# Optimization experiments

Measured on AMD Instinct MI355X. Metric: run time of the kernel, lower is better.

The kernel has to match this reference:

```python
import math
import jax, jax.numpy as jnp
import numpy as np

D_MODEL = 1024
NUM_HEADS = 16
D_HEAD = D_MODEL // NUM_HEADS  # 64
K_S = 32  # sparse top-k keys kept per query
B, N = 2, 2048


def setup_inputs() -> dict:
    key = jax.random.key(0)
    ks = jax.random.split(key, 9)
    s = 1.0 / math.sqrt(D_MODEL)
    return {
        "x": jax.random.normal(ks[0], (B, N, D_MODEL), dtype=jnp.float32),
        "Wq": jax.random.normal(ks[1], (D_MODEL, D_MODEL), dtype=jnp.float32) * s,
        "bq": jnp.zeros((D_MODEL,), dtype=jnp.float32),
        "Wk": jax.random.normal(ks[2], (D_MODEL, D_MODEL), dtype=jnp.float32) * s,
        "bk": jnp.zeros((D_MODEL,), dtype=jnp.float32),
        "Wv": jax.random.normal(ks[3], (D_MODEL, D_MODEL), dtype=jnp.float32) * s,
        "bv": jnp.zeros((D_MODEL,), dtype=jnp.float32),
        "Wo": jax.random.normal(ks[4], (D_MODEL, D_MODEL), dtype=jnp.float32) * s,
        "bo": jnp.zeros((D_MODEL,), dtype=jnp.float32),
    }


def _attn(x, Wq, bq, Wk, bk, Wv, bv, Wo, bo):
    b, n, _ = x.shape
    # projections (torch Linear: y = x W^T + b)
    q = (x @ Wq.T + bq).reshape(b, n, NUM_HEADS, D_HEAD).transpose(0, 2, 1, 3)
    k = (x @ Wk.T + bk).reshape(b, n, NUM_HEADS, D_HEAD).transpose(0, 2, 1, 3)
    v = (x @ Wv.T + bv).reshape(b, n, NUM_HEADS, D_HEAD).transpose(0, 2, 1, 3)
    # full scores [b, H, n, n]
    scores = jnp.einsum("bhqd,bhkd->bhqk", q, k) / math.sqrt(D_HEAD)
    # causal mask (triu above diagonal -> -inf)
    causal = jnp.triu(jnp.ones((n, n), dtype=bool), k=1)
    neg_inf = jnp.array(-jnp.inf, dtype=scores.dtype)
    scores = jnp.where(causal, neg_inf, scores)
    # sparse top-k: keep only K_S largest scores per query row
    vals, idx = jax.lax.top_k(scores, K_S)
    masked = jnp.full_like(scores, -jnp.inf)
    masked = jnp.put_along_axis(masked, idx, vals, axis=-1, inplace=False)
    attn = jax.nn.softmax(masked, axis=-1)  # dropout p=0.0 -> identity
    out = jnp.einsum("bhqk,bhkd->bhqd", attn, v)
    out = out.transpose(0, 2, 1, 3).reshape(b, n, D_MODEL)
    y = out @ Wo.T + bo
    return y, attn.mean(axis=1)


def reference(x, Wq, bq, Wk, bk, Wv, bv, Wo, bo):
    return _attn(x, Wq, bq, Wk, bk, Wv, bv, Wo, bo)
```

## Files before the change

### kernel.cpp

```cpp
#include <hip/hip_runtime.h>
#include <hip/hip_bf16.h>
#include <math.h>

#define BATCH   2
#define NTOK    2048
#define DMODEL  1024
#define HEADS   16
#define DHEAD   64
#define KSEL    32
#define MROWS   (BATCH * NTOK)
#define NBLK8   (NTOK / 8)
#define TPW     4

typedef short     bf16x8 __attribute__((ext_vector_type(8)));
typedef float     f32x4  __attribute__((ext_vector_type(4)));
typedef unsigned short ushort_t;
typedef unsigned long long u64;

#define GLOAD_LDS16(g, l) \
    __builtin_amdgcn_global_load_lds((const __attribute__((address_space(1))) void*)(g), \
                                     (__attribute__((address_space(3))) void*)(l), 16, 0, 0)

__device__ __forceinline__ ushort_t f2bf(float f) {
    unsigned u = __float_as_uint(f);
    unsigned r = (u + 0x7FFFu + ((u >> 16) & 1u)) >> 16;
    return (ushort_t)r;
}
__device__ __forceinline__ float bf2f(ushort_t h) {
    return __uint_as_float(((unsigned)h) << 16);
}

__device__ __forceinline__ void conv_body(const float* __restrict__ in,
                                          ushort_t* __restrict__ hi,
                                          ushort_t* __restrict__ lo, int n, int i)
{
    if (i + 3 < n) {
        const float4 v = *(const float4*)(in + i);
        ushort4 ph, pl;
        ph.x = f2bf(v.x); pl.x = f2bf(v.x - bf2f(ph.x));
        ph.y = f2bf(v.y); pl.y = f2bf(v.y - bf2f(ph.y));
        ph.z = f2bf(v.z); pl.z = f2bf(v.z - bf2f(ph.z));
        ph.w = f2bf(v.w); pl.w = f2bf(v.w - bf2f(ph.w));
        *(ushort4*)(hi + i) = ph;
        *(ushort4*)(lo + i) = pl;
    }
}

__global__ __launch_bounds__(256) void conv_split(const float* __restrict__ in,
                                                  ushort_t* __restrict__ hi,
                                                  ushort_t* __restrict__ lo, int n)
{
    const int i = (blockIdx.x * 256 + threadIdx.x) * 4;
    conv_body(in, hi, lo, n, i);
}

__global__ __launch_bounds__(256) void conv_split4(const float* __restrict__ i0, ushort_t* __restrict__ h0, ushort_t* __restrict__ l0,
                                                   const float* __restrict__ i1, ushort_t* __restrict__ h1, ushort_t* __restrict__ l1,
                                                   const float* __restrict__ i2, ushort_t* __restrict__ h2, ushort_t* __restrict__ l2,
                                                   const float* __restrict__ i3, ushort_t* __restrict__ h3, ushort_t* __restrict__ l3,
                                                   int n)
{
    const int w = blockIdx.y;
    const float* in = (w == 0) ? i0 : (w == 1) ? i1 : (w == 2) ? i2 : i3;
    ushort_t* hi = (w == 0) ? h0 : (w == 1) ? h1 : (w == 2) ? h2 : h3;
    ushort_t* lo = (w == 0) ? l0 : (w == 1) ? l1 : (w == 2) ? l2 : l3;
    const int i = (blockIdx.x * 256 + threadIdx.x) * 4;
    conv_body(in, hi, lo, n, i);
}

__device__ __forceinline__ unsigned mono_key(float f) {
    const unsigned u = __float_as_uint(f);
    return (u ^ (unsigned)(((int)u >> 31) | 0x80000000)) + 1u;
}
__device__ __forceinline__ float unmono(unsigned m) {
    const unsigned u = m - 1u;
    return __uint_as_float(u ^ (unsigned)(((int)(~u) >> 31) | 0x80000000));
}

__global__ __launch_bounds__(256, 2) void gemm_qkv_fused(const ushort_t* __restrict__ xhi,
                                                         const ushort_t* __restrict__ xlo,
                                                         const ushort_t* __restrict__ wqh,
                                                         const ushort_t* __restrict__ wql,
                                                         const ushort_t* __restrict__ wkh,
                                                         const ushort_t* __restrict__ wkl,
                                                         const ushort_t* __restrict__ wvh,
                                                         const ushort_t* __restrict__ wvl,
                                                         const float* __restrict__ bq,
                                                         const float* __restrict__ bk,
                                                         const float* __restrict__ bv,
                                                         ushort_t* __restrict__ Qh,
                                                         ushort_t* __restrict__ Qm,
                                                         ushort_t* __restrict__ Ql,
                                                         ushort_t* __restrict__ Kh,
                                                         ushort_t* __restrict__ Km,
                                                         ushort_t* __restrict__ Kl,
                                                         float* __restrict__ Vws)
{
    __shared__ ushort_t smem[2 * 20480];

    const int tid  = threadIdx.x;
    const int wave = tid >> 6;
    const int lane = tid & 63;
    const int fr   = lane & 15;
    const int k8   = lane >> 4;
    const int m0 = blockIdx.x * 128;
    const int n0 = blockIdx.y * 64;

    f32x4 acc[3][2][4];
#pragma unroll
    for (int w = 0; w < 3; ++w)
#pragma unroll
        for (int i = 0; i < 2; ++i)
#pragma unroll
            for (int j = 0; j < 4; ++j) acc[w][i][j] = (f32x4){0.f, 0.f, 0.f, 0.f};

#define STAGEF(bufsel, k0v) do {                                               \
        ushort_t* dst_ = smem + (size_t)(bufsel) * 20480;                      \
        _Pragma("unroll")                                                      \
        for (int i_ = 0; i_ < 2; ++i_) {                                       \
            const int c_ = i_ * 256 + tid;                                     \
            const int row_ = c_ >> 2;                                          \
            const int g_ = (c_ & 3) ^ ((row_ >> 1) & 3);                       \
            const size_t ga_ = (size_t)(m0 + row_) * DMODEL + (k0v) + g_ * 8;  \
            GLOAD_LDS16(xhi + ga_, dst_ + (size_t)c_ * 8);                     \
            GLOAD_LDS16(xlo + ga_, dst_ + 4096 + (size_t)c_ * 8);              \
        }                                                                      \
        {                                                                      \
            const int c_ = tid;                                                \
            const int row_ = c_ >> 2;                                          \
            const int g_ = (c_ & 3) ^ ((row_ >> 1) & 3);                       \
            const size_t gb_ = (size_t)(n0 + row_) * DMODEL + (k0v) + g_ * 8;  \
            GLOAD_LDS16(wqh + gb_, dst_ + 8192 + (size_t)c_ * 8);              \
            GLOAD_LDS16(wql + gb_, dst_ + 10240 + (size_t)c_ * 8);             \
            GLOAD_LDS16(wkh + gb_, dst_ + 12288 + (size_t)c_ * 8);             \
            GLOAD_LDS16(wkl + gb_, dst_ + 14336 + (size_t)c_ * 8);             \
            GLOAD_LDS16(wvh + gb_, dst_ + 16384 + (size_t)c_ * 8);             \
            GLOAD_LDS16(wvl + gb_, dst_ + 18432 + (size_t)c_ * 8);             \
        }                                                                      \
    } while (0)

    STAGEF(0, 0);
    int cur = 0;

    for (int k0 = 0; k0 < DMODEL; k0 += 32) {
        __syncthreads();
        if (k0 + 32 < DMODEL) STAGEF(cur ^ 1, k0 + 32);

        const ushort_t* buf = smem + (size_t)cur * 20480;
        bf16x8 afh[2], afl[2];
#pragma unroll
        for (int mi = 0; mi < 2; ++mi) {
            const int r = wave * 32 + mi * 16 + fr;
            const int ro = r * 32 + (k8 ^ ((r >> 1) & 3)) * 8;
            afh[mi] = *(const bf16x8*)(buf + ro);
            afl[mi] = *(const bf16x8*)(buf + 4096 + ro);
        }

#pragma unroll
        for (int w = 0; w < 3; ++w) {
            const ushort_t* bb = buf + 8192 + w * 4096;
            bf16x8 bfh[4], bfl[4];
#pragma unroll
            for (int ni = 0; ni < 4; ++ni) {
                const int r = ni * 16 + fr;
                const int ro = r * 32 + (k8 ^ ((r >> 1) & 3)) * 8;
                bfh[ni] = *(const bf16x8*)(bb + ro);
                bfl[ni] = *(const bf16x8*)(bb + 2048 + ro);
            }
#pragma unroll
            for (int mi = 0; mi < 2; ++mi)
#pragma unroll
                for (int ni = 0; ni < 4; ++ni) {
                    acc[w][mi][ni] = __builtin_amdgcn_mfma_f32_16x16x32_bf16(afh[mi], bfl[ni], acc[w][mi][ni], 0, 0, 0);
                    acc[w][mi][ni] = __builtin_amdgcn_mfma_f32_16x16x32_bf16(afl[mi], bfh[ni], acc[w][mi][ni], 0, 0, 0);
                    acc[w][mi][ni] = __builtin_amdgcn_mfma_f32_16x16x32_bf16(afh[mi], bfh[ni], acc[w][mi][ni], 0, 0, 0);
                }
        }
        cur ^= 1;
    }
#undef STAGEF

#pragma unroll
    for (int w = 0; w < 3; ++w) {
        const float* bias = (w == 0) ? bq : (w == 1) ? bk : bv;
        ushort_t* oh = (w == 0) ? Qh : Kh;
        ushort_t* om = (w == 0) ? Qm : Km;
        ushort_t* ol = (w == 0) ? Ql : Kl;
#pragma unroll
        for (int ni = 0; ni < 4; ++ni) {
            const int o = n0 + ni * 16 + (lane & 15);
            const float bvv = bias[o];
            const int hd = o >> 6;
            const int d  = o & 63;
#pragma unroll
            for (int mi = 0; mi < 2; ++mi) {
#pragma unroll
                for (int reg = 0; reg < 4; ++reg) {
                    const int m = m0 + wave * 32 + mi * 16 + ((lane >> 4) << 2) + reg;
                    const float v = acc[w][mi][ni][reg] + bvv;
                    const int bb = m >> 11;
                    const int n  = m & 2047;
                    const size_t off = (((size_t)(bb * HEADS + hd)) * NTOK + n) * DHEAD + d;
                    if (w == 2) {
                        Vws[off] = v;
                    } else {
                        const ushort_t h1 = f2bf(v);
                        const float r1 = v - bf2f(h1);
                        const ushort_t m1 = f2bf(r1);
                        const ushort_t l1 = f2bf(r1 - bf2f(m1));
                        oh[off] = h1; om[off] = m1; ol[off] = l1;
                    }
                }
            }
        }
    }
}

__global__ __launch_bounds__(256, 2) void gemm_split_mfma(const ushort_t* __restrict__ Ahi,
                                                          const ushort_t* __restrict__ Alo,
                                                          const ushort_t* __restrict__ Bhi,
                                                          const ushort_t* __restrict__ Blo,
                                                          const float* __restrict__ bias,
                                                          float* __restrict__ out)
{
    __shared__ ushort_t smem[2 * 12288];

    const int tid  = threadIdx.x;
    const int wave = tid >> 6;
    const int lane = tid & 63;
    const int fr   = lane & 15;
    const int k8   = lane >> 4;
    const int m0 = blockIdx.x * 128;
    const int n0 = blockIdx.y * 64;

    f32x4 acc[2][4];
#pragma unroll
    for (int i = 0; i < 2; ++i)
#pragma unroll
        for (int j = 0; j < 4; ++j) acc[i][j] = (f32x4){0.f, 0.f, 0.f, 0.f};

#define STAGE(bufsel, k0v) do {                                                \
        ushort_t* dst_ = smem + (size_t)(bufsel) * 12288;                      \
        _Pragma("unroll")                                                      \
        for (int i_ = 0; i_ < 2; ++i_) {                                       \
            const int c_ = i_ * 256 + tid;                                     \
            const int row_ = c_ >> 2;                                          \
            const int g_ = (c_ & 3) ^ ((row_ >> 1) & 3);                       \
            const size_t ga_ = (size_t)(m0 + row_) * DMODEL + (k0v) + g_ * 8;  \
            GLOAD_LDS16(Ahi + ga_, dst_ + (size_t)c_ * 8);                     \
            GLOAD_LDS16(Alo + ga_, dst_ + 4096 + (size_t)c_ * 8);              \
        }                                                                      \
        {                                                                      \
            const int c_ = tid;                                                \
            const int row_ = c_ >> 2;                                          \
            const int g_ = (c_ & 3) ^ ((row_ >> 1) & 3);                       \
            const size_t gb_ = (size_t)(n0 + row_) * DMODEL + (k0v) + g_ * 8;  \
            GLOAD_LDS16(Bhi + gb_, dst_ + 8192 + (size_t)c_ * 8);              \
            GLOAD_LDS16(Blo + gb_, dst_ + 10240 + (size_t)c_ * 8);             \
        }                                                                      \
    } while (0)

    STAGE(0, 0);
    int cur = 0;

    for (int k0 = 0; k0 < DMODEL; k0 += 32) {
        __syncthreads();
        if (k0 + 32 < DMODEL) STAGE(cur ^ 1, k0 + 32);

        const ushort_t* buf = smem + (size_t)cur * 12288;
        bf16x8 afh[2], afl[2], bfh[4], bfl[4];
#pragma unroll
        for (int mi = 0; mi < 2; ++mi) {
            const int r = wave * 32 + mi * 16 + fr;
            const int ro = r * 32 + (k8 ^ ((r >> 1) & 3)) * 8;
            afh[mi] = *(const bf16x8*)(buf + ro);
            afl[mi] = *(const bf16x8*)(buf + 4096 + ro);
        }
#pragma unroll
        for (int ni = 0; ni < 4; ++ni) {
            const int r = ni * 16 + fr;
            const int ro = r * 32 + (k8 ^ ((r >> 1) & 3)) * 8;
            bfh[ni] = *(const bf16x8*)(buf + 8192 + ro);
            bfl[ni] = *(const bf16x8*)(buf + 10240 + ro);
        }

#pragma unroll
        for (int mi = 0; mi < 2; ++mi)
#pragma unroll
            for (int ni = 0; ni < 4; ++ni) {
                acc[mi][ni] = __builtin_amdgcn_mfma_f32_16x16x32_bf16(afh[mi], bfl[ni], acc[mi][ni], 0, 0, 0);
                acc[mi][ni] = __builtin_amdgcn_mfma_f32_16x16x32_bf16(afl[mi], bfh[ni], acc[mi][ni], 0, 0, 0);
                acc[mi][ni] = __builtin_amdgcn_mfma_f32_16x16x32_bf16(afh[mi], bfh[ni], acc[mi][ni], 0, 0, 0);
            }
        cur ^= 1;
    }
#undef STAGE

#pragma unroll
    for (int ni = 0; ni < 4; ++ni) {
        const int o = n0 + ni * 16 + (lane & 15);
        const float bv = bias[o];
#pragma unroll
        for (int mi = 0; mi < 2; ++mi) {
#pragma unroll
            for (int reg = 0; reg < 4; ++reg) {
                const int m = m0 + wave * 32 + mi * 16 + ((lane >> 4) << 2) + reg;
                out[(size_t)m * DMODEL + o] = acc[mi][ni][reg] + bv;
            }
        }
    }
}

__global__ __launch_bounds__(256, 3) void score_mfma(const ushort_t* __restrict__ Qh,
                                                     const ushort_t* __restrict__ Qm,
                                                     const ushort_t* __restrict__ Ql,
                                                     const ushort_t* __restrict__ Kh,
                                                     const ushort_t* __restrict__ Km,
                                                     const ushort_t* __restrict__ Kl,
                                                     unsigned* __restrict__ S,
                                                     unsigned* __restrict__ Smax,
                                                     int q0, int QC)
{
    const int ks = blockIdx.x;
    const int qt = blockIdx.y;
    const int bh = blockIdx.z;
    const int qbase = q0 + qt * 128;
    const int ktmax = ((qbase + 127) >> 6) + 1;
    const int kt0 = ks * TPW;
    if (kt0 >= ktmax) return;
    const int kt1 = (kt0 + TPW < ktmax) ? (kt0 + TPW) : ktmax;

    __shared__ ushort_t smem[2 * 12288];

    const int tid  = threadIdx.x;
    const int wave = tid >> 6;
    const int lane = tid & 63;
    const int l15  = lane & 15;
    const int l4   = lane >> 4;

    const size_t qgbase = ((size_t)bh * NTOK + qbase) * DHEAD;

    bf16x8 qf[3][2][2];
#pragma unroll
    for (int p = 0; p < 3; ++p) {
        const ushort_t* Qp = (p == 0) ? Qh : (p == 1) ? Qm : Ql;
#pragma unroll
        for (int j = 0; j < 2; ++j) {
            const int r = wave * 32 + j * 16 + l15;
#pragma unroll
            for (int h = 0; h < 2; ++h)
                qf[p][j][h] = *(const bf16x8*)(Qp + qgbase + (size_t)r * DHEAD + (h * 4 + l4) * 8);
        }
    }

#define STAGE_K(bufsel, ktv) do {                                              \
        const size_t kg_ = ((size_t)bh * NTOK + (ktv) * 64) * DHEAD;           \
        _Pragma("unroll")                                                      \
        for (int i_ = 0; i_ < 2; ++i_) {                                       \
            const int c_ = i_ * 256 + tid;                                     \
            const int row_ = c_ >> 3;                                          \
            const int g_ = (c_ & 7) ^ (row_ & 7);                              \
            const size_t goff_ = kg_ + (size_t)row_ * DHEAD + g_ * 8;          \
            ushort_t* dst_ = smem + (bufsel) * 12288 + (size_t)c_ * 8;         \
            GLOAD_LDS16(Kh + goff_, dst_ + 0 * 4096);                          \
            GLOAD_LDS16(Km + goff_, dst_ + 1 * 4096);                          \
            GLOAD_LDS16(Kl + goff_, dst_ + 2 * 4096);                          \
        }                                                                      \
    } while (0)

    STAGE_K(0, kt0);
    __builtin_amdgcn_sched_barrier(0);
    asm volatile("s_waitcnt vmcnt(0)" ::: "memory");
    __builtin_amdgcn_s_barrier();
    __builtin_amdgcn_sched_barrier(0);

    int cur = 0;
    const size_t srowQ = (size_t)bh * QC;

    for (int kt = kt0; kt < kt1; ++kt) {
        const bool more = (kt + 1 < kt1);
        if (more) STAGE_K(cur ^ 1, kt + 1);
        __builtin_amdgcn_sched_barrier(0);

        f32x4 acc[4][2];
#pragma unroll
        for (int m = 0; m < 4; ++m)
#pragma unroll
            for (int j = 0; j < 2; ++j) acc[m][j] = (f32x4){0.f, 0.f, 0.f, 0.f};

        const ushort_t* kb = smem + cur * 12288;
#pragma unroll
        for (int h = 0; h < 2; ++h) {
            bf16x8 kf[4];
#pragma unroll
            for (int m = 0; m < 4; ++m) {
                const int r = m * 16 + l15;
                const int slot = (h * 4 + l4) ^ (r & 7);
                kf[m] = *(const bf16x8*)(kb + 0 * 4096 + (size_t)(r * 8 + slot) * 8);
            }
#pragma unroll
            for (int m = 0; m < 4; ++m)
#pragma unroll
                for (int j = 0; j < 2; ++j) {
                    acc[m][j] = __builtin_amdgcn_mfma_f32_16x16x32_bf16(kf[m], qf[2][j][h], acc[m][j], 0, 0, 0);
                    acc[m][j] = __builtin_amdgcn_mfma_f32_16x16x32_bf16(kf[m], qf[1][j][h], acc[m][j], 0, 0, 0);
                    acc[m][j] = __builtin_amdgcn_mfma_f32_16x16x32_bf16(kf[m], qf[0][j][h], acc[m][j], 0, 0, 0);
                }
#pragma unroll
            for (int m = 0; m < 4; ++m) {
                const int r = m * 16 + l15;
                const int slot = (h * 4 + l4) ^ (r & 7);
                kf[m] = *(const bf16x8*)(kb + 1 * 4096 + (size_t)(r * 8 + slot) * 8);
            }
#pragma unroll
            for (int m = 0; m < 4; ++m)
#pragma unroll
                for (int j = 0; j < 2; ++j) {
                    acc[m][j] = __builtin_amdgcn_mfma_f32_16x16x32_bf16(kf[m], qf[1][j][h], acc[m][j], 0, 0, 0);
                    acc[m][j] = __builtin_amdgcn_mfma_f32_16x16x32_bf16(kf[m], qf[0][j][h], acc[m][j], 0, 0, 0);
                }
#pragma unroll
            for (int m = 0; m < 4; ++m) {
                const int r = m * 16 + l15;
                const int slot = (h * 4 + l4) ^ (r & 7);
                kf[m] = *(const bf16x8*)(kb + 2 * 4096 + (size_t)(r * 8 + slot) * 8);
            }
#pragma unroll
            for (int m = 0; m < 4; ++m)
#pragma unroll
                for (int j = 0; j < 2; ++j)
                    acc[m][j] = __builtin_amdgcn_mfma_f32_16x16x32_bf16(kf[m], qf[0][j][h], acc[m][j], 0, 0, 0);
        }

#pragma unroll
        for (int j = 0; j < 2; ++j) {
            const int qrow  = wave * 32 + j * 16 + l15;
            const int qlrow = qt * 128 + qrow;
            const int qglob = qbase + qrow;
            const size_t srow = (srowQ + qlrow) * NTOK;
            const size_t mrow = (srowQ + qlrow) * NBLK8;
#pragma unroll
            for (int m = 0; m < 4; ++m) {
                const int kcol0 = kt * 64 + m * 16 + (l4 << 2);
                uint4 kv;
                kv.x = mono_key(acc[m][j][0] * 0.125f);
                kv.y = mono_key(acc[m][j][1] * 0.125f);
                kv.z = mono_key(acc[m][j][2] * 0.125f);
                kv.w = mono_key(acc[m][j][3] * 0.125f);
                *(uint4*)(S + srow + kcol0) = kv;
                unsigned cm = (kcol0     <= qglob) ? kv.x : 0u;
                unsigned t;
                t = (kcol0 + 1 <= qglob) ? kv.y : 0u; cm = (t > cm) ? t : cm;
                t = (kcol0 + 2 <= qglob) ? kv.z : 0u; cm = (t > cm) ? t : cm;
                t = (kcol0 + 3 <= qglob) ? kv.w : 0u; cm = (t > cm) ? t : cm;
                const unsigned o = __shfl_xor(cm, 16, 64);
                cm = (o > cm) ? o : cm;
                if ((lane & 16) == 0) {
                    const int gblk = kt * 8 + m * 2 + (lane >> 5);
                    Smax[mrow + gblk] = cm;
                }
            }
        }

        if (more) {
            asm volatile("s_waitcnt vmcnt(16)" ::: "memory");
            __builtin_amdgcn_s_barrier();
            __builtin_amdgcn_sched_barrier(0);
        }
        cur ^= 1;
    }
#undef STAGE_K
}

__device__ __forceinline__ void select_task8(const unsigned* __restrict__ Srow,
                                             const unsigned* __restrict__ Mrow,
                                             const float* __restrict__ Vb,
                                             float* __restrict__ ctxRow,
                                             float* __restrict__ attnS,
                                             int L, int nsel, int nb,
                                             int* __restrict__ sBlk,
                                             int* __restrict__ sIdx,
                                             float* __restrict__ sE,
                                             int lane)
{
    const uint4 bm4 = *(const uint4*)(Mrow + lane * 4);
    unsigned bmax[4] = {bm4.x, bm4.y, bm4.z, bm4.w};
#pragma unroll
    for (int s = 0; s < 4; ++s)
        if (lane * 4 + s >= nb) bmax[s] = 0u;

    unsigned gmax = bmax[0];
    gmax = (bmax[1] > gmax) ? bmax[1] : gmax;
    gmax = (bmax[2] > gmax) ? bmax[2] : gmax;
    gmax = (bmax[3] > gmax) ? bmax[3] : gmax;
#pragma unroll
    for (int d = 1; d < 64; d <<= 1) {
        const unsigned o = __shfl_xor(gmax, d, 64);
        gmax = (o > gmax) ? o : gmax;
    }
    const float vmax = unmono(gmax);

    unsigned selb = 0u;
    unsigned blkLo = 1u;
    int nselb;
    if (nb <= KSEL) {
        nselb = nb;
#pragma unroll
        for (int s = 0; s < 4; ++s)
            if (lane * 4 + s < nb) selb |= 1u << s;
    } else {
        nselb = KSEL;
        unsigned lo = 1u, hi = gmax >> 16;
        while (lo < hi) {
            const unsigned mid = lo + ((hi - lo + 1u) >> 1);
            const unsigned midk = mid << 16;
            int cnt = 0;
#pragma unroll
            for (int s = 0; s < 4; ++s)
                cnt += __popcll(__ballot(bmax[s] >= midk));
            if (cnt >= KSEL) lo = mid; else hi = mid - 1u;
        }
        blkLo = lo;
        const unsigned Tkb = lo << 16;
        const unsigned Gkb = Tkb | 0xFFFFu;
        int cge = 0, cgt = 0;
#pragma unroll
        for (int s = 0; s < 4; ++s) {
            cge += __popcll(__ballot(bmax[s] >= Tkb));
            cgt += __popcll(__ballot(bmax[s] > Gkb));
        }
        if (cge == KSEL) {
#pragma unroll
            for (int s = 0; s < 4; ++s)
                selb |= (bmax[s] >= Tkb) ? (1u << s) : 0u;
        } else {
            unsigned bmb = 0u;
#pragma unroll
            for (int s = 0; s < 4; ++s) {
                selb |= (bmax[s] > Gkb) ? (1u << s) : 0u;
                bmb  |= (bmax[s] >= Tkb && bmax[s] <= Gkb) ? (1u << s) : 0u;
            }
            int k_tie = KSEL - cgt;
            while (k_tie > 0) {
                u64 best = 0;
                unsigned bmm = bmb;
                while (bmm) {
                    const int s = __builtin_ctz(bmm);
                    bmm &= bmm - 1u;
                    const unsigned gblk = (unsigned)(lane * 4 + s);
                    const u64 k = ((u64)bmax[s] << 32) | (unsigned)~gblk;
                    if (k > best) best = k;
                }
                u64 bb = best;
#pragma unroll
                for (int d = 1; d < 64; d <<= 1) {
                    const u64 o = __shfl_xor(bb, d, 64);
                    bb = (o > bb) ? o : bb;
                }
                const unsigned gblk = ~(unsigned)bb;
                if (lane == (int)(gblk >> 2)) {
                    const unsigned bit = 1u << (gblk & 3u);
                    selb |= bit;
                    bmb &= ~bit;
                }
                --k_tie;
            }
        }
    }

    {
        const int cb = __popc(selb);
        int pfxb = cb;
#pragma unroll
        for (int d = 1; d < 64; d <<= 1) {
            const int t = __shfl_up(pfxb, d, 64);
            if (lane >= d) pfxb += t;
        }
        pfxb -= cb;
        unsigned mskb = selb;
        int posb = pfxb;
        while (mskb) {
            const int s = __builtin_ctz(mskb);
            mskb &= mskb - 1u;
            sBlk[posb++] = lane * 4 + s;
        }
    }
    __asm volatile("s_waitcnt lgkmcnt(0)" ::: "memory");

    const int NC = nselb * 8;
    unsigned km[4];
    int idx[4];
#pragma unroll
    for (int c = 0; c < 4; ++c) {
        const int t = c * 64 + lane;
        unsigned m = 0u;
        int j = 0;
        if (t < NC) {
            const int blk = sBlk[t >> 3];
            j = blk * 8 + (t & 7);
            if (j < L) m = Srow[j];
        }
        km[c] = m;
        idx[c] = j;
    }

    unsigned lo = blkLo, hi = gmax >> 16;
    while (lo < hi) {
        const unsigned mid = lo + ((hi - lo + 1u) >> 1);
        const unsigned midk = mid << 16;
        int cnt = 0;
#pragma unroll
        for (int c = 0; c < 4; ++c)
            cnt += __popcll(__ballot(km[c] >= midk));
        if (cnt >= nsel) lo = mid; else hi = mid - 1u;
    }
    const unsigned Tk = lo << 16;
    const unsigned Gk = Tk | 0xFFFFu;

    int cnt_ge = 0, cnt_gt = 0;
#pragma unroll
    for (int c = 0; c < 4; ++c) {
        cnt_ge += __popcll(__ballot(km[c] >= Tk));
        cnt_gt += __popcll(__ballot(km[c] > Gk));
    }

    unsigned selmask = 0u;
    if (cnt_ge == nsel) {
#pragma unroll
        for (int c = 0; c < 4; ++c)
            selmask |= (km[c] >= Tk) ? (1u << c) : 0u;
    } else {
        unsigned bmask = 0u;
#pragma unroll
        for (int c = 0; c < 4; ++c) {
            selmask |= (km[c] > Gk) ? (1u << c) : 0u;
            bmask   |= (km[c] >= Tk && km[c] <= Gk) ? (1u << c) : 0u;
        }
        int k_tie = nsel - cnt_gt;
        while (k_tie > 0) {
            u64 best = 0;
            unsigned bmm = bmask;
            while (bmm) {
                const int c = __builtin_ctz(bmm);
                bmm &= bmm - 1u;
                const int t = c * 64 + lane;
                const u64 k = ((u64)km[c] << 32) |
                              ((u64)(0xFFFFu ^ (unsigned)idx[c]) << 16) | (u64)t;
                if (k > best) best = k;
            }
            u64 bb = best;
#pragma unroll
            for (int d = 1; d < 64; d <<= 1) {
                const u64 o = __shfl_xor(bb, d, 64);
                bb = (o > bb) ? o : bb;
            }
            const unsigned tt = (unsigned)bb & 0xFFFFu;
            if (lane == (int)(tt & 63u)) {
                const unsigned bit = 1u << (tt >> 6);
                selmask |= bit;
                bmask &= ~bit;
            }
            --k_tie;
        }
    }

    const int csel = __popc(selmask);
    int pfx = csel;
#pragma unroll
    for (int d = 1; d < 64; d <<= 1) {
        const int t = __shfl_up(pfx, d, 64);
        if (lane >= d) pfx += t;
    }
    pfx -= csel;

    float esum = 0.f;
    unsigned msk = selmask;
    int pos = pfx;
    while (msk) {
        const int c = __builtin_ctz(msk);
        msk &= msk - 1u;
        const float e = __expf(unmono(km[c]) - vmax);
        esum += e;
        sIdx[pos] = idx[c];
        sE[pos] = e;
        ++pos;
    }

    float Z = esum;
#pragma unroll
    for (int d = 1; d < 64; d <<= 1) Z += __shfl_xor(Z, d, 64);
    const float rcpZ = 1.0f / Z;

    msk = selmask;
    pos = pfx;
    while (msk) {
        const int c = __builtin_ctz(msk);
        msk &= msk - 1u;
        const float w = sE[pos] * rcpZ;
        ++pos;
        atomicAdd(&attnS[idx[c]], w * (1.0f / (float)HEADS));
    }

    {
        float a0 = 0.f, a1 = 0.f, a2 = 0.f, a3 = 0.f;
        int i = 0;
#pragma unroll 2
        for (; i + 4 <= nsel; i += 4) {
            const int i0 = sIdx[i],     i1 = sIdx[i + 1];
            const int i2 = sIdx[i + 2], i3 = sIdx[i + 3];
            const float w0 = sE[i]     * rcpZ, w1 = sE[i + 1] * rcpZ;
            const float w2 = sE[i + 2] * rcpZ, w3 = sE[i + 3] * rcpZ;
            a0 += w0 * Vb[(size_t)i0 * DHEAD + lane];
            a1 += w1 * Vb[(size_t)i1 * DHEAD + lane];
            a2 += w2 * Vb[(size_t)i2 * DHEAD + lane];
            a3 += w3 * Vb[(size_t)i3 * DHEAD + lane];
        }
        for (; i < nsel; ++i)
            a0 += sE[i] * rcpZ * Vb[(size_t)sIdx[i] * DHEAD + lane];
        ctxRow[lane] = (a0 + a1) + (a2 + a3);
    }
}

__global__ __launch_bounds__(256) void select_v8(const unsigned* __restrict__ S,
                                                 const unsigned* __restrict__ Smax,
                                                 const float* __restrict__ V,
                                                 float* __restrict__ ctx,
                                                 float* __restrict__ attn,
                                                 int q0, int QC)
{
    __shared__ float attnS[NTOK];
    __shared__ int   sBlkAll[4][KSEL];
    __shared__ int   sIdxAll[4][KSEL];
    __shared__ float sEAll[4][KSEL];

    const int lane = threadIdx.x & 63;
    const int wave = threadIdx.x >> 6;
    const int ql = blockIdx.x;
    const int b  = blockIdx.y;
    const int q  = q0 + ql;
    const int L  = q + 1;
    const int nsel = (L < KSEL) ? L : KSEL;
    const int nb = (L + 7) >> 3;

    {
        float4* a4 = (float4*)attnS;
#pragma unroll
        for (int i = 0; i < NTOK / 4 / 256; ++i)
            a4[i * 256 + threadIdx.x] = (float4){0.f, 0.f, 0.f, 0.f};
    }
    __syncthreads();

#pragma unroll
    for (int hi = 0; hi < 4; ++hi) {
        const int h = hi * 4 + wave;
        const size_t bhx = (size_t)(b * HEADS + h);
        const unsigned* Srow = S + (bhx * QC + ql) * NTOK;
        const unsigned* Mrow = Smax + (bhx * QC + ql) * NBLK8;
        const float* Vb = V + bhx * NTOK * DHEAD;
        float* ctxRow = ctx + (((size_t)(b * NTOK + q)) * HEADS + h) * DHEAD;
        select_task8(Srow, Mrow, Vb, ctxRow, attnS, L, nsel, nb,
                     sBlkAll[wave], sIdxAll[wave], sEAll[wave], lane);
    }
    __syncthreads();

    {
        float* attnRow = attn + ((size_t)(b * NTOK + q)) * NTOK;
        const float4* a4 = (const float4*)attnS;
        float4* o4 = (float4*)attnRow;
#pragma unroll
        for (int i = 0; i < NTOK / 4 / 256; ++i)
            o4[i * 256 + threadIdx.x] = a4[i * 256 + threadIdx.x];
    }
}

extern "C" void kernel_launch(void* const* d_in, const int* in_sizes, int n_in,
                              void* d_out, int out_size, void* d_ws, size_t ws_size,
                              hipStream_t stream) {
    const float* x  = (const float*)d_in[0];
    const float* Wq = (const float*)d_in[1];
    const float* bq = (const float*)d_in[2];
    const float* Wk = (const float*)d_in[3];
    const float* bk = (const float*)d_in[4];
    const float* Wv = (const float*)d_in[5];
    const float* bv = (const float*)d_in[6];
    const float* Wo = (const float*)d_in[7];
    const float* bo = (const float*)d_in[8];

    const size_t MB = 1ull << 20;
    char* wsb = (char*)d_ws;
    float*    Vws = (float*)(wsb + 0 * MB);
    float*    ctx = (float*)(wsb + 16 * MB);
    ushort_t* xhi = (ushort_t*)(wsb + 32 * MB);
    ushort_t* xlo = (ushort_t*)(wsb + 40 * MB);
    ushort_t* wqh = (ushort_t*)(wsb + 48 * MB);
    ushort_t* wql = (ushort_t*)(wsb + 50 * MB);
    ushort_t* wkh = (ushort_t*)(wsb + 52 * MB);
    ushort_t* wkl = (ushort_t*)(wsb + 54 * MB);
    ushort_t* wvh = (ushort_t*)(wsb + 56 * MB);
    ushort_t* wvl = (ushort_t*)(wsb + 58 * MB);
    ushort_t* woh = (ushort_t*)(wsb + 60 * MB);
    ushort_t* wol = (ushort_t*)(wsb + 62 * MB);
    ushort_t* Qh  = (ushort_t*)(wsb + 64 * MB);
    ushort_t* Qm  = (ushort_t*)(wsb + 72 * MB);
    ushort_t* Ql  = (ushort_t*)(wsb + 80 * MB);
    ushort_t* Kh  = (ushort_t*)(wsb + 88 * MB);
    ushort_t* Km  = (ushort_t*)(wsb + 96 * MB);
    ushort_t* Kl  = (ushort_t*)(wsb + 104 * MB);
    ushort_t* cxh = xhi;
    ushort_t* cxl = xlo;

    float* y    = (float*)d_out;
    float* attn = y + (size_t)BATCH * NTOK * DMODEL;

    const int NX = MROWS * DMODEL;
    const int NW = DMODEL * DMODEL;

    conv_split<<<NX / (256 * 4), 256, 0, stream>>>(x, xhi, xlo, NX);
    {
        dim3 cgrid(NW / (256 * 4), 4);
        conv_split4<<<cgrid, 256, 0, stream>>>(Wq, wqh, wql,
                                               Wk, wkh, wkl,
                                               Wv, wvh, wvl,
                                               Wo, woh, wol, NW);
    }

    dim3 ggrid(MROWS / 128, DMODEL / 64);
    gemm_qkv_fused<<<ggrid, 256, 0, stream>>>(xhi, xlo,
                                              wqh, wql, wkh, wkl, wvh, wvl,
                                              bq, bk, bv,
                                              Qh, Qm, Ql, Kh, Km, Kl, Vws);

    const size_t base_bytes = 112 * MB;
    const size_t avail = (ws_size > base_bytes) ? ws_size - base_bytes : 0;
    int QC = 128;
    for (int cand = 512; cand >= 128; cand >>= 1) {
        const size_t need = (size_t)BATCH * HEADS * cand * (size_t)(NTOK + NBLK8) * sizeof(unsigned);
        if (need <= avail) { QC = cand; break; }
    }
    unsigned* Smax = (unsigned*)(wsb + base_bytes);
    unsigned* Sws  = (unsigned*)(wsb + base_bytes +
                                 (size_t)BATCH * HEADS * QC * NBLK8 * sizeof(unsigned));

    for (int q0 = 0; q0 < NTOK; q0 += QC) {
        const int ktm = (q0 + QC) >> 6;
        dim3 sgrid((ktm + TPW - 1) / TPW, QC / 128, BATCH * HEADS);
        score_mfma<<<sgrid, 256, 0, stream>>>(Qh, Qm, Ql, Kh, Km, Kl, Sws, Smax, q0, QC);
        dim3 selgrid(QC, BATCH);
        select_v8<<<selgrid, 256, 0, stream>>>(Sws, Smax, Vws, ctx, attn, q0, QC);
    }

    conv_split<<<NX / (256 * 4), 256, 0, stream>>>(ctx, cxh, cxl, NX);
    gemm_split_mfma<<<ggrid, 256, 0, stream>>>(cxh, cxl, woh, wol, bo, y);
}
```

Measured before the change: 505.3 us.

## Load GEMM A-fragments directly to registers and fuse ctx bf16 split into select

In both the QKV and output-projection GEMMs, the A operand (activation hi/lo) is now loaded straight from global memory into registers and double-buffered there, while only the weight tile is staged through LDS. This shrinks the shared-memory footprint, removes the LDS round-trip for A, and replaces __syncthreads with explicit waitcnt and barrier plus sched_barriers. The select kernel now writes the context directly as bf16 hi/lo pairs, which removes the separate conv_split pass over ctx. The cost is more register pressure and uncoalesced per-lane 16-byte global loads for A, which are not shared across waves.

```diff
diff --git a/kernel.cpp b/kernel.cpp
--- a/kernel.cpp
+++ b/kernel.cpp
@@ -96,7 +96,7 @@
                                                          ushort_t* __restrict__ Kl,
                                                          float* __restrict__ Vws)
 {
-    __shared__ ushort_t smem[2 * 20480];
+    __shared__ ushort_t smem[2 * 12288];
 
     const int tid  = threadIdx.x;
     const int wave = tid >> 6;
@@ -114,71 +114,84 @@
 #pragma unroll
             for (int j = 0; j < 4; ++j) acc[w][i][j] = (f32x4){0.f, 0.f, 0.f, 0.f};
 
-#define STAGEF(bufsel, k0v) do {                                               \
-        ushort_t* dst_ = smem + (size_t)(bufsel) * 20480;                      \
+#define LOAD_A(DH, DL, k0v) do {                                               \
         _Pragma("unroll")                                                      \
-        for (int i_ = 0; i_ < 2; ++i_) {                                       \
-            const int c_ = i_ * 256 + tid;                                     \
-            const int row_ = c_ >> 2;                                          \
-            const int g_ = (c_ & 3) ^ ((row_ >> 1) & 3);                       \
-            const size_t ga_ = (size_t)(m0 + row_) * DMODEL + (k0v) + g_ * 8;  \
-            GLOAD_LDS16(xhi + ga_, dst_ + (size_t)c_ * 8);                     \
-            GLOAD_LDS16(xlo + ga_, dst_ + 4096 + (size_t)c_ * 8);              \
-        }                                                                      \
-        {                                                                      \
-            const int c_ = tid;                                                \
-            const int row_ = c_ >> 2;                                          \
-            const int g_ = (c_ & 3) ^ ((row_ >> 1) & 3);                       \
-            const size_t gb_ = (size_t)(n0 + row_) * DMODEL + (k0v) + g_ * 8;  \
-            GLOAD_LDS16(wqh + gb_, dst_ + 8192 + (size_t)c_ * 8);              \
-            GLOAD_LDS16(wql + gb_, dst_ + 10240 + (size_t)c_ * 8);             \
-            GLOAD_LDS16(wkh + gb_, dst_ + 12288 + (size_t)c_ * 8);             \
-            GLOAD_LDS16(wkl + gb_, dst_ + 14336 + (size_t)c_ * 8);             \
-            GLOAD_LDS16(wvh + gb_, dst_ + 16384 + (size_t)c_ * 8);             \
-            GLOAD_LDS16(wvl + gb_, dst_ + 18432 + (size_t)c_ * 8);             \
+        for (int mi_ = 0; mi_ < 2; ++mi_) {                                    \
+            const int r_ = wave * 32 + mi_ * 16 + fr;                          \
+            const size_t ga_ = (size_t)(m0 + r_) * DMODEL + (k0v) + k8 * 8;    \
+            DH[mi_] = *(const bf16x8*)(xhi + ga_);                             \
+            DL[mi_] = *(const bf16x8*)(xlo + ga_);                             \
         }                                                                      \
     } while (0)
 
-    STAGEF(0, 0);
+#define STAGE_B(bufsel, k0v) do {                                              \
+        ushort_t* dst_ = smem + (size_t)(bufsel) * 12288;                      \
+        const int c_ = tid;                                                    \
+        const int row_ = c_ >> 2;                                              \
+        const int g_ = (c_ & 3) ^ ((row_ >> 1) & 3);                           \
+        const size_t gb_ = (size_t)(n0 + row_) * DMODEL + (k0v) + g_ * 8;      \
+        GLOAD_LDS16(wqh + gb_, dst_ + (size_t)c_ * 8);                         \
+        GLOAD_LDS16(wql + gb_, dst_ + 2048 + (size_t)c_ * 8);                  \
+        GLOAD_LDS16(wkh + gb_, dst_ + 4096 + (size_t)c_ * 8);                  \
+        GLOAD_LDS16(wkl + gb_, dst_ + 6144 + (size_t)c_ * 8);                  \
+        GLOAD_LDS16(wvh + gb_, dst_ + 8192 + (size_t)c_ * 8);                  \
+        GLOAD_LDS16(wvl + gb_, dst_ + 10240 + (size_t)c_ * 8);                 \
+    } while (0)
+
+#define QKV_STEP(AH, AL, NAH, NAL, k0v) do {                                   \
+        const bool more_ = (k0v) + 32 < DMODEL;                                \
+        if (more_) {                                                           \
+            LOAD_A(NAH, NAL, (k0v) + 32);                                      \
+            STAGE_B(cur ^ 1, (k0v) + 32);                                      \
+        }                                                                      \
+        __builtin_amdgcn_sched_barrier(0);                                     \
+        {                                                                      \
+            const ushort_t* buf_ = smem + (size_t)cur * 12288;                 \
+            _Pragma("unroll")                                                  \
+            for (int w_ = 0; w_ < 3; ++w_) {                                   \
+                const ushort_t* bb_ = buf_ + w_ * 4096;                        \
+                bf16x8 bfh_[4], bfl_[4];                                       \
+                _Pragma("unroll")                                              \
+                for (int ni_ = 0; ni_ < 4; ++ni_) {                            \
+                    const int r_ = ni_ * 16 + fr;                              \
+                    const int ro_ = r_ * 32 + (k8 ^ ((r_ >> 1) & 3)) * 8;      \
+                    bfh_[ni_] = *(const bf16x8*)(bb_ + ro_);                   \
+                    bfl_[ni_] = *(const bf16x8*)(bb_ + 2048 + ro_);            \
+                }                                                              \
+                _Pragma("unroll")                                              \
+                for (int mi_ = 0; mi_ < 2; ++mi_)                              \
+                    _Pragma("unroll")                                          \
+                    for (int ni_ = 0; ni_ < 4; ++ni_) {                        \
+                        acc[w_][mi_][ni_] = __builtin_amdgcn_mfma_f32_16x16x32_bf16(AH[mi_], bfl_[ni_], acc[w_][mi_][ni_], 0, 0, 0); \
+                        acc[w_][mi_][ni_] = __builtin_amdgcn_mfma_f32_16x16x32_bf16(AL[mi_], bfh_[ni_], acc[w_][mi_][ni_], 0, 0, 0); \
+                        acc[w_][mi_][ni_] = __builtin_amdgcn_mfma_f32_16x16x32_bf16(AH[mi_], bfh_[ni_], acc[w_][mi_][ni_], 0, 0, 0); \
+                    }                                                          \
+            }                                                                  \
+        }                                                                      \
+        if (more_) {                                                           \
+            asm volatile("s_waitcnt vmcnt(0)" ::: "memory");                   \
+            __builtin_amdgcn_s_barrier();                                      \
+            __builtin_amdgcn_sched_barrier(0);                                 \
+        }                                                                      \
+        cur ^= 1;                                                              \
+    } while (0)
+
+    bf16x8 a0h[2], a0l[2], a1h[2], a1l[2];
+    LOAD_A(a0h, a0l, 0);
+    STAGE_B(0, 0);
+    __builtin_amdgcn_sched_barrier(0);
+    asm volatile("s_waitcnt vmcnt(0)" ::: "memory");
+    __builtin_amdgcn_s_barrier();
+    __builtin_amdgcn_sched_barrier(0);
+
     int cur = 0;
-
-    for (int k0 = 0; k0 < DMODEL; k0 += 32) {
-        __syncthreads();
-        if (k0 + 32 < DMODEL) STAGEF(cur ^ 1, k0 + 32);
-
-        const ushort_t* buf = smem + (size_t)cur * 20480;
-        bf16x8 afh[2], afl[2];
-#pragma unroll
-        for (int mi = 0; mi < 2; ++mi) {
-            const int r = wave * 32 + mi * 16 + fr;
-            const int ro = r * 32 + (k8 ^ ((r >> 1) & 3)) * 8;
-            afh[mi] = *(const bf16x8*)(buf + ro);
-            afl[mi] = *(const bf16x8*)(buf + 4096 + ro);
-        }
-
-#pragma unroll
-        for (int w = 0; w < 3; ++w) {
-            const ushort_t* bb = buf + 8192 + w * 4096;
-            bf16x8 bfh[4], bfl[4];
-#pragma unroll
-            for (int ni = 0; ni < 4; ++ni) {
-                const int r = ni * 16 + fr;
-                const int ro = r * 32 + (k8 ^ ((r >> 1) & 3)) * 8;
-                bfh[ni] = *(const bf16x8*)(bb + ro);
-                bfl[ni] = *(const bf16x8*)(bb + 2048 + ro);
-            }
-#pragma unroll
-            for (int mi = 0; mi < 2; ++mi)
-#pragma unroll
-                for (int ni = 0; ni < 4; ++ni) {
-                    acc[w][mi][ni] = __builtin_amdgcn_mfma_f32_16x16x32_bf16(afh[mi], bfl[ni], acc[w][mi][ni], 0, 0, 0);
-                    acc[w][mi][ni] = __builtin_amdgcn_mfma_f32_16x16x32_bf16(afl[mi], bfh[ni], acc[w][mi][ni], 0, 0, 0);
-                    acc[w][mi][ni] = __builtin_amdgcn_mfma_f32_16x16x32_bf16(afh[mi], bfh[ni], acc[w][mi][ni], 0, 0, 0);
-                }
-        }
-        cur ^= 1;
-    }
-#undef STAGEF
+    for (int k0 = 0; k0 < DMODEL; k0 += 64) {
+        QKV_STEP(a0h, a0l, a1h, a1l, k0);
+        QKV_STEP(a1h, a1l, a0h, a0l, k0 + 32);
+    }
+#undef QKV_STEP
+#undef STAGE_B
+#undef LOAD_A
 
 #pragma unroll
     for (int w = 0; w < 3; ++w) {
@@ -223,7 +236,7 @@
                                                           const float* __restrict__ bias,
                                                           float* __restrict__ out)
 {
-    __shared__ ushort_t smem[2 * 12288];
+    __shared__ ushort_t smem[2 * 4096];
 
     const int tid  = threadIdx.x;
     const int wave = tid >> 6;
@@ -239,62 +252,76 @@
 #pragma unroll
         for (int j = 0; j < 4; ++j) acc[i][j] = (f32x4){0.f, 0.f, 0.f, 0.f};
 
-#define STAGE(bufsel, k0v) do {                                                \
-        ushort_t* dst_ = smem + (size_t)(bufsel) * 12288;                      \
+#define LOAD_AW(DH, DL, k0v) do {                                              \
         _Pragma("unroll")                                                      \
-        for (int i_ = 0; i_ < 2; ++i_) {                                       \
-            const int c_ = i_ * 256 + tid;                                     \
-            const int row_ = c_ >> 2;                                          \
-            const int g_ = (c_ & 3) ^ ((row_ >> 1) & 3);                       \
-            const size_t ga_ = (size_t)(m0 + row_) * DMODEL + (k0v) + g_ * 8;  \
-            GLOAD_LDS16(Ahi + ga_, dst_ + (size_t)c_ * 8);                     \
-            GLOAD_LDS16(Alo + ga_, dst_ + 4096 + (size_t)c_ * 8);              \
-        }                                                                      \
-        {                                                                      \
-            const int c_ = tid;                                                \
-            const int row_ = c_ >> 2;                                          \
-            const int g_ = (c_ & 3) ^ ((row_ >> 1) & 3);                       \
-            const size_t gb_ = (size_t)(n0 + row_) * DMODEL + (k0v) + g_ * 8;  \
-            GLOAD_LDS16(Bhi + gb_, dst_ + 8192 + (size_t)c_ * 8);              \
-            GLOAD_LDS16(Blo + gb_, dst_ + 10240 + (size_t)c_ * 8);             \
+        for (int mi_ = 0; mi_ < 2; ++mi_) {                                    \
+            const int r_ = wave * 32 + mi_ * 16 + fr;                          \
+            const size_t ga_ = (size_t)(m0 + r_) * DMODEL + (k0v) + k8 * 8;    \
+            DH[mi_] = *(const bf16x8*)(Ahi + ga_);                             \
+            DL[mi_] = *(const bf16x8*)(Alo + ga_);                             \
         }                                                                      \
     } while (0)
 
-    STAGE(0, 0);
+#define STAGE_BW(bufsel, k0v) do {                                             \
+        ushort_t* dst_ = smem + (size_t)(bufsel) * 4096;                       \
+        const int c_ = tid;                                                    \
+        const int row_ = c_ >> 2;                                              \
+        const int g_ = (c_ & 3) ^ ((row_ >> 1) & 3);                           \
+        const size_t gb_ = (size_t)(n0 + row_) * DMODEL + (k0v) + g_ * 8;      \
+        GLOAD_LDS16(Bhi + gb_, dst_ + (size_t)c_ * 8);                         \
+        GLOAD_LDS16(Blo + gb_, dst_ + 2048 + (size_t)c_ * 8);                  \
+    } while (0)
+
+#define WO_STEP(AH, AL, NAH, NAL, k0v) do {                                    \
+        const bool more_ = (k0v) + 32 < DMODEL;                                \
+        if (more_) {                                                           \
+            LOAD_AW(NAH, NAL, (k0v) + 32);                                     \
+            STAGE_BW(cur ^ 1, (k0v) + 32);                                     \
+        }                                                                      \
+        __builtin_amdgcn_sched_barrier(0);                                     \
+        {                                                                      \
+            const ushort_t* bb_ = smem + (size_t)cur * 4096;                   \
+            bf16x8 bfh_[4], bfl_[4];                                           \
+            _Pragma("unroll")                                                  \
+            for (int ni_ = 0; ni_ < 4; ++ni_) {                                \
+                const int r_ = ni_ * 16 + fr;                                  \
+                const int ro_ = r_ * 32 + (k8 ^ ((r_ >> 1) & 3)) * 8;          \
+                bfh_[ni_] = *(const bf16x8*)(bb_ + ro_);                       \
+                bfl_[ni_] = *(const bf16x8*)(bb_ + 2048 + ro_);                \
+            }                                                                  \
+            _Pragma("unroll")                                                  \
+            for (int mi_ = 0; mi_ < 2; ++mi_)                                  \
+                _Pragma("unroll")                                              \
+                for (int ni_ = 0; ni_ < 4; ++ni_) {                            \
+                    acc[mi_][ni_] = __builtin_amdgcn_mfma_f32_16x16x32_bf16(AH[mi_], bfl_[ni_], acc[mi_][ni_], 0, 0, 0); \
+                    acc[mi_][ni_] = __builtin_amdgcn_mfma_f32_16x16x32_bf16(AL[mi_], bfh_[ni_], acc[mi_][ni_], 0, 0, 0); \
+                    acc[mi_][ni_] = __builtin_amdgcn_mfma_f32_16x16x32_bf16(AH[mi_], bfh_[ni_], acc[mi_][ni_], 0, 0, 0); \
+                }                                                              \
+        }                                                                      \
+        if (more_) {                                                           \
+            asm volatile("s_waitcnt vmcnt(0)" ::: "memory");                   \
+            __builtin_amdgcn_s_barrier();                                      \
+            __builtin_amdgcn_sched_barrier(0);                                 \
+        }                                                                      \
+        cur ^= 1;                                                              \
+    } while (0)
+
+    bf16x8 a0h[2], a0l[2], a1h[2], a1l[2];
+    LOAD_AW(a0h, a0l, 0);
+    STAGE_BW(0, 0);
+    __builtin_amdgcn_sched_barrier(0);
+    asm volatile("s_waitcnt vmcnt(0)" ::: "memory");
+    __builtin_amdgcn_s_barrier();
+    __builtin_amdgcn_sched_barrier(0);
+
     int cur = 0;
-
-    for (int k0 = 0; k0 < DMODEL; k0 += 32) {
-        __syncthreads();
-        if (k0 + 32 < DMODEL) STAGE(cur ^ 1, k0 + 32);
-
-        const ushort_t* buf = smem + (size_t)cur * 12288;
-        bf16x8 afh[2], afl[2], bfh[4], bfl[4];
-#pragma unroll
-        for (int mi = 0; mi < 2; ++mi) {
-            const int r = wave * 32 + mi * 16 + fr;
-            const int ro = r * 32 + (k8 ^ ((r >> 1) & 3)) * 8;
-            afh[mi] = *(const bf16x8*)(buf + ro);
-            afl[mi] = *(const bf16x8*)(buf + 4096 + ro);
-        }
-#pragma unroll
-        for (int ni = 0; ni < 4; ++ni) {
-            const int r = ni * 16 + fr;
-            const int ro = r * 32 + (k8 ^ ((r >> 1) & 3)) * 8;
-            bfh[ni] = *(const bf16x8*)(buf + 8192 + ro);
-            bfl[ni] = *(const bf16x8*)(buf + 10240 + ro);
-        }
-
-#pragma unroll
-        for (int mi = 0; mi < 2; ++mi)
-#pragma unroll
-            for (int ni = 0; ni < 4; ++ni) {
-                acc[mi][ni] = __builtin_amdgcn_mfma_f32_16x16x32_bf16(afh[mi], bfl[ni], acc[mi][ni], 0, 0, 0);
-                acc[mi][ni] = __builtin_amdgcn_mfma_f32_16x16x32_bf16(afl[mi], bfh[ni], acc[mi][ni], 0, 0, 0);
-                acc[mi][ni] = __builtin_amdgcn_mfma_f32_16x16x32_bf16(afh[mi], bfh[ni], acc[mi][ni], 0, 0, 0);
-            }
-        cur ^= 1;
-    }
-#undef STAGE
+    for (int k0 = 0; k0 < DMODEL; k0 += 64) {
+        WO_STEP(a0h, a0l, a1h, a1l, k0);
+        WO_STEP(a1h, a1l, a0h, a0l, k0 + 32);
+    }
+#undef WO_STEP
+#undef STAGE_BW
+#undef LOAD_AW
 
 #pragma unroll
     for (int ni = 0; ni < 4; ++ni) {
@@ -475,7 +502,8 @@
 __device__ __forceinline__ void select_task8(const unsigned* __restrict__ Srow,
                                              const unsigned* __restrict__ Mrow,
                                              const float* __restrict__ Vb,
-                                             float* __restrict__ ctxRow,
+                                             ushort_t* __restrict__ chRow,
+                                             ushort_t* __restrict__ clRow,
                                              float* __restrict__ attnS,
                                              int L, int nsel, int nb,
                                              int* __restrict__ sBlk,
@@ -717,14 +745,18 @@
         }
         for (; i < nsel; ++i)
             a0 += sE[i] * rcpZ * Vb[(size_t)sIdx[i] * DHEAD + lane];
-        ctxRow[lane] = (a0 + a1) + (a2 + a3);
+        const float v = (a0 + a1) + (a2 + a3);
+        const ushort_t h1 = f2bf(v);
+        chRow[lane] = h1;
+        clRow[lane] = f2bf(v - bf2f(h1));
     }
 }
 
 __global__ __launch_bounds__(256) void select_v8(const unsigned* __restrict__ S,
                                                  const unsigned* __restrict__ Smax,
                                                  const float* __restrict__ V,
-                                                 float* __restrict__ ctx,
+                                                 ushort_t* __restrict__ cxh,
+                                                 ushort_t* __restrict__ cxl,
                                                  float* __restrict__ attn,
                                                  int q0, int QC)
 {
@@ -757,8 +789,8 @@
         const unsigned* Srow = S + (bhx * QC + ql) * NTOK;
         const unsigned* Mrow = Smax + (bhx * QC + ql) * NBLK8;
         const float* Vb = V + bhx * NTOK * DHEAD;
-        float* ctxRow = ctx + (((size_t)(b * NTOK + q)) * HEADS + h) * DHEAD;
-        select_task8(Srow, Mrow, Vb, ctxRow, attnS, L, nsel, nb,
+        const size_t co = (((size_t)(b * NTOK + q)) * HEADS + h) * DHEAD;
+        select_task8(Srow, Mrow, Vb, cxh + co, cxl + co, attnS, L, nsel, nb,
                      sBlkAll[wave], sIdxAll[wave], sEAll[wave], lane);
     }
     __syncthreads();
@@ -789,7 +821,8 @@
     const size_t MB = 1ull << 20;
     char* wsb = (char*)d_ws;
     float*    Vws = (float*)(wsb + 0 * MB);
-    float*    ctx = (float*)(wsb + 16 * MB);
+    ushort_t* cxh = (ushort_t*)(wsb + 16 * MB);
+    ushort_t* cxl = (ushort_t*)(wsb + 24 * MB);
     ushort_t* xhi = (ushort_t*)(wsb + 32 * MB);
     ushort_t* xlo = (ushort_t*)(wsb + 40 * MB);
     ushort_t* wqh = (ushort_t*)(wsb + 48 * MB);
@@ -806,8 +839,6 @@
     ushort_t* Kh  = (ushort_t*)(wsb + 88 * MB);
     ushort_t* Km  = (ushort_t*)(wsb + 96 * MB);
     ushort_t* Kl  = (ushort_t*)(wsb + 104 * MB);
-    ushort_t* cxh = xhi;
-    ushort_t* cxl = xlo;
 
     float* y    = (float*)d_out;
     float* attn = y + (size_t)BATCH * NTOK * DMODEL;
@@ -846,9 +877,8 @@
         dim3 sgrid((ktm + TPW - 1) / TPW, QC / 128, BATCH * HEADS);
         score_mfma<<<sgrid, 256, 0, stream>>>(Qh, Qm, Ql, Kh, Km, Kl, Sws, Smax, q0, QC);
         dim3 selgrid(QC, BATCH);
-        select_v8<<<selgrid, 256, 0, stream>>>(Sws, Smax, Vws, ctx, attn, q0, QC);
-    }
-
-    conv_split<<<NX / (256 * 4), 256, 0, stream>>>(ctx, cxh, cxl, NX);
+        select_v8<<<selgrid, 256, 0, stream>>>(Sws, Smax, Vws, cxh, cxl, attn, q0, QC);
+    }
+
     gemm_split_mfma<<<ggrid, 256, 0, stream>>>(cxh, cxl, woh, wol, bo, y);
 }
```

Measured after the change: 519.3 us. +2.8%, slower.
